# Kernel tuning notes

Hardware: AMD Instinct MI355X
Metric: run time of the kernel (lower is better)

Reference implementation:

```python
import jax, jax.numpy as jnp
import numpy as np

N_NODES = 50000
N_EDGES = 640000
HIDDEN = 128
EDGE_FEATS = 16
NUM_LAYERS = 4
NUM_GRAPHS = 64
LN_EPS = 1e-5


def setup_inputs() -> dict:
    key = jax.random.key(0)
    ks = jax.random.split(key, 12)
    s = 1.0 / np.sqrt(HIDDEN)
    se = 1.0 / np.sqrt(EDGE_FEATS)
    return {
        "x": jax.random.normal(ks[0], (N_NODES, HIDDEN), jnp.float32),
        "batch_index": jnp.sort(jax.random.randint(ks[1], (N_NODES,), 0, NUM_GRAPHS)),
        "edge_index": jax.random.randint(ks[2], (2, N_EDGES), 0, N_NODES),
        "edge_attr": jax.random.normal(ks[3], (N_EDGES, EDGE_FEATS), jnp.float32),
        # edge_transform Linear(EDGE_FEATS -> HIDDEN)
        "We": jax.random.uniform(ks[4], (EDGE_FEATS, HIDDEN), jnp.float32, -se, se),
        "be": jax.random.uniform(ks[5], (HIDDEN,), jnp.float32, -se, se),
        # per-layer GINE MLP: Linear-ReLU-Linear, stacked over layers
        "W1": jax.random.uniform(ks[6], (NUM_LAYERS, HIDDEN, HIDDEN), jnp.float32, -s, s),
        "b1": jax.random.uniform(ks[7], (NUM_LAYERS, HIDDEN), jnp.float32, -s, s),
        "W2": jax.random.uniform(ks[8], (NUM_LAYERS, HIDDEN, HIDDEN), jnp.float32, -s, s),
        "b2": jax.random.uniform(ks[9], (NUM_LAYERS, HIDDEN), jnp.float32, -s, s),
        # per-layer LayerNorm params
        "ln_g": jnp.ones((NUM_LAYERS, HIDDEN), jnp.float32),
        "ln_b": jnp.zeros((NUM_LAYERS, HIDDEN), jnp.float32),
    }


def reference(x, batch_index, edge_index, edge_attr, We, be, W1, b1, W2, b2, ln_g, ln_b):
    n = x.shape[0]
    src, dst = edge_index[0], edge_index[1]
    ea = edge_attr @ We + be  # [E, H] shared across layers
    h = x
    for l in range(W1.shape[0]):
        # GINEConv message: ReLU(x_j + edge_attr), scatter-sum at dst
        m = jax.nn.relu(h[src] + ea)
        agg = jax.ops.segment_sum(m, dst, num_segments=n)
        z = h + agg  # (1 + eps) * x + agg with eps = 0
        z = jax.nn.relu(z @ W1[l] + b1[l]) @ W2[l] + b2[l]
        # LayerNorm over feature dim
        mu = jnp.mean(z, axis=-1, keepdims=True)
        var = jnp.var(z, axis=-1, keepdims=True)
        z = (z - mu) / jnp.sqrt(var + LN_EPS) * ln_g[l] + ln_b[l]
        # dropout(p=0) is identity
        h = jax.nn.relu(z) + h
    return h
```

## Files before the change

### kernel.cpp

```cpp
#include <hip/hip_runtime.h>

#define HIDDEN 128
#define NLAYERS 4

typedef __attribute__((ext_vector_type(8))) short short8;
typedef __attribute__((ext_vector_type(4))) float f32x4;

__device__ __forceinline__ ushort f2bf(float f) {
    uint x = __builtin_bit_cast(uint, f);
    return (ushort)((x + 0x7fffu + ((x >> 16) & 1u)) >> 16);
}
__device__ __forceinline__ float bflo(uint u) {
    return __builtin_bit_cast(float, u << 16);
}
__device__ __forceinline__ float bfhi(uint u) {
    return __builtin_bit_cast(float, u & 0xffff0000u);
}


__global__ void hist_kernel(const int* __restrict__ dst, int* __restrict__ counts, int E) {
    int e = blockIdx.x * blockDim.x + threadIdx.x;
    if (e < E) atomicAdd(&counts[dst[e]], 1);
}

__global__ __launch_bounds__(1024) void scan_kernel(const int* __restrict__ counts,
                                                    int* __restrict__ offsets,
                                                    int* __restrict__ wpos, int n) {
    __shared__ int wsum[16];
    __shared__ int carry_s;
    const int t = threadIdx.x, wv = t >> 6, ln = t & 63;
    if (t == 0) carry_s = 0;
    __syncthreads();
    for (int base = 0; base < n; base += 4096) {
        const int i = base + t * 4;
        int4 c = {0, 0, 0, 0};
        if (i + 3 < n) {
            c = *(const int4*)(counts + i);
        } else {
            if (i < n)     c.x = counts[i];
            if (i + 1 < n) c.y = counts[i + 1];
            if (i + 2 < n) c.z = counts[i + 2];
            if (i + 3 < n) c.w = counts[i + 3];
        }
        const int tsum = c.x + c.y + c.z + c.w;
        int s = tsum;
#pragma unroll
        for (int off = 1; off < 64; off <<= 1) {
            int x = __shfl_up(s, off, 64);
            if (ln >= off) s += x;
        }
        if (ln == 63) wsum[wv] = s;
        __syncthreads();
        if (t < 16) {
            int x = wsum[t];
#pragma unroll
            for (int off = 1; off < 16; off <<= 1) {
                int y = __shfl_up(x, off, 16);
                if ((t & 15) >= off) x += y;
            }
            wsum[t] = x;
        }
        __syncthreads();
        const int wbase = (wv ? wsum[wv - 1] : 0) + carry_s;
        const int excl = wbase + s - tsum;
        int4 o;
        o.x = excl;
        o.y = excl + c.x;
        o.z = o.y + c.y;
        o.w = o.z + c.z;
        if (i + 3 < n) {
            *(int4*)(offsets + i) = o;
            *(int4*)(wpos + i) = o;
        } else {
            if (i < n)     { offsets[i] = o.x;     wpos[i] = o.x; }
            if (i + 1 < n) { offsets[i + 1] = o.y; wpos[i + 1] = o.y; }
            if (i + 2 < n) { offsets[i + 2] = o.z; wpos[i + 2] = o.z; }
            if (i + 3 < n) { offsets[i + 3] = o.w; wpos[i + 3] = o.w; }
        }
        __syncthreads();
        if (t == 0) carry_s += wsum[15];
        __syncthreads();
    }
    if (t == 0) offsets[n] = carry_s;
}

__global__ void fill_kernel(const int* __restrict__ src, const int* __restrict__ dst,
                            int* __restrict__ wpos, int* __restrict__ csr_src,
                            int* __restrict__ csr_eid, int E) {
    int e = blockIdx.x * blockDim.x + threadIdx.x;
    if (e < E) {
        int d = dst[e];
        int p = atomicAdd(&wpos[d], 1);
        csr_src[p] = src[e];
        csr_eid[p] = e;
    }
}


__global__ void h16init_kernel(const float* __restrict__ x, ushort* __restrict__ h16p, int total) {
    int i = blockIdx.x * blockDim.x + threadIdx.x;
    if (i < total) {
        int row = i >> 4, lm = i & 15;
        const float* xp = x + (size_t)row * HIDDEN + lm;
        uint4 o;
        o.x = (uint)f2bf(xp[0])  | ((uint)f2bf(xp[16]) << 16);
        o.y = (uint)f2bf(xp[32]) | ((uint)f2bf(xp[48]) << 16);
        o.z = (uint)f2bf(xp[64]) | ((uint)f2bf(xp[80]) << 16);
        o.w = (uint)f2bf(xp[96]) | ((uint)f2bf(xp[112]) << 16);
        *(uint4*)(h16p + (size_t)row * HIDDEN + lm * 8) = o;
    }
}

__global__ void wconv_kernel(const float* __restrict__ W1, const float* __restrict__ W2,
                             ushort* __restrict__ Wt) {
    int i = blockIdx.x * blockDim.x + threadIdx.x;
    int l = i >> 15;
    int m = (i >> 14) & 1;
    int nn = (i >> 7) & 127;
    int kpos = i & 127;
    int kk = (m == 0) ? (((kpos & 7) << 4) | (kpos >> 3)) : kpos;
    const float* W = m ? W2 : W1;
    Wt[i] = f2bf(W[l * 16384 + kk * 128 + nn]);
}

__global__ void wecol_kernel(const float* __restrict__ We, ushort* __restrict__ Wecol) {
    int i = blockIdx.x * blockDim.x + threadIdx.x;
    if (i < 128 * 16) {
        int ch = i >> 4, f = i & 15;
        Wecol[i] = f2bf(We[f * HIDDEN + ch]);
    }
}

__global__ void eattr16_kernel(const int* __restrict__ csr_eid,
                               const float4* __restrict__ edge_attr,
                               ushort* __restrict__ eattr16, int total4) {
    int i = blockIdx.x * blockDim.x + threadIdx.x;
    if (i < total4) {
        int p = i >> 2, part = i & 3;
        int eid = csr_eid[p];
        float4 v = edge_attr[(size_t)eid * 4 + part];
        uint2 o;
        o.x = (uint)f2bf(v.x) | ((uint)f2bf(v.y) << 16);
        o.y = (uint)f2bf(v.z) | ((uint)f2bf(v.w) << 16);
        *(uint2*)(eattr16 + (size_t)p * 16 + part * 4) = o;
    }
}

__global__ __launch_bounds__(256) void agg_kernel(const ushort* __restrict__ h16p,
                                                  const float* __restrict__ h32,
                                                  const int* __restrict__ csr_src,
                                                  const ushort* __restrict__ eattr16,
                                                  const int* __restrict__ offsets,
                                                  const ushort* __restrict__ Wecol,
                                                  const float* __restrict__ be,
                                                  ushort* __restrict__ z0p, int n) {
    const int w = threadIdx.x >> 6, l = threadIdx.x & 63;
    const int v = blockIdx.x * 4 + w;
    if (v >= n) return;
    const int lm = l & 15, lg = l >> 4;

    short8 bfr[8];
    float bev[8];
#pragma unroll
    for (int nt = 0; nt < 8; ++nt) {
        if (lg < 2) bfr[nt] = *(const short8*)(Wecol + (nt * 16 + lm) * 16 + lg * 8);
        else        bfr[nt] = short8{0, 0, 0, 0, 0, 0, 0, 0};
        bev[nt] = be[nt * 16 + lm];
    }

    const int e0 = offsets[v], e1 = offsets[v + 1];
    float acc[8];
#pragma unroll
    for (int i = 0; i < 8; ++i) acc[i] = 0.f;

    for (int B = e0; B < e1; B += 16) {
        short8 af = short8{0, 0, 0, 0, 0, 0, 0, 0};
        if (lg < 2) {
            int ae = B + lm;
            if (ae >= e1) ae = e1 - 1;
            af = *(const short8*)(eattr16 + (size_t)ae * 16 + lg * 8);
        }

        int ecs[4];
        float vm[4];
#pragma unroll
        for (int j = 0; j < 4; ++j) {
            int e = B + lg * 4 + j;
            vm[j] = (e < e1) ? 1.f : 0.f;
            ecs[j] = (e < e1) ? e : (e1 - 1);
        }
        int sj[4];
#pragma unroll
        for (int j = 0; j < 4; ++j) sj[j] = csr_src[ecs[j]];
        uint4 hv[4];
#pragma unroll
        for (int j = 0; j < 4; ++j)
            hv[j] = *(const uint4*)(h16p + (size_t)sj[j] * HIDDEN + lm * 8);

        f32x4 d[8];
#pragma unroll
        for (int nt = 0; nt < 8; ++nt) {
            f32x4 c = {bev[nt], bev[nt], bev[nt], bev[nt]};
            d[nt] = __builtin_amdgcn_mfma_f32_16x16x32_bf16(af, bfr[nt], c, 0, 0, 0);
        }

#pragma unroll
        for (int j = 0; j < 4; ++j) {
            float hc0 = bflo(hv[j].x), hc1 = bfhi(hv[j].x);
            float hc2 = bflo(hv[j].y), hc3 = bfhi(hv[j].y);
            float hc4 = bflo(hv[j].z), hc5 = bfhi(hv[j].z);
            float hc6 = bflo(hv[j].w), hc7 = bfhi(hv[j].w);
            acc[0] = fmaf(vm[j], fmaxf(d[0][j] + hc0, 0.f), acc[0]);
            acc[1] = fmaf(vm[j], fmaxf(d[1][j] + hc1, 0.f), acc[1]);
            acc[2] = fmaf(vm[j], fmaxf(d[2][j] + hc2, 0.f), acc[2]);
            acc[3] = fmaf(vm[j], fmaxf(d[3][j] + hc3, 0.f), acc[3]);
            acc[4] = fmaf(vm[j], fmaxf(d[4][j] + hc4, 0.f), acc[4]);
            acc[5] = fmaf(vm[j], fmaxf(d[5][j] + hc5, 0.f), acc[5]);
            acc[6] = fmaf(vm[j], fmaxf(d[6][j] + hc6, 0.f), acc[6]);
            acc[7] = fmaf(vm[j], fmaxf(d[7][j] + hc7, 0.f), acc[7]);
        }
    }

#pragma unroll
    for (int i = 0; i < 8; ++i) {
        acc[i] += __shfl_xor(acc[i], 16, 64);
        acc[i] += __shfl_xor(acc[i], 32, 64);
    }

    if (lg == 0) {
        const float* hp = h32 + (size_t)v * HIDDEN + lm;
        float s0 = hp[0]   + acc[0], s1 = hp[16]  + acc[1];
        float s2 = hp[32]  + acc[2], s3 = hp[48]  + acc[3];
        float s4 = hp[64]  + acc[4], s5 = hp[80]  + acc[5];
        float s6 = hp[96]  + acc[6], s7 = hp[112] + acc[7];
        uint4 o;
        o.x = (uint)f2bf(s0) | ((uint)f2bf(s1) << 16);
        o.y = (uint)f2bf(s2) | ((uint)f2bf(s3) << 16);
        o.z = (uint)f2bf(s4) | ((uint)f2bf(s5) << 16);
        o.w = (uint)f2bf(s6) | ((uint)f2bf(s7) << 16);
        *(uint4*)(z0p + (size_t)v * HIDDEN + lm * 8) = o;
    }
}

__global__ __launch_bounds__(256, 3) void mlp_kernel(const ushort* __restrict__ z0p,
                                                     float* __restrict__ h32,
                                                     ushort* __restrict__ h16p,
                                                     const ushort* __restrict__ W1t,
                                                     const ushort* __restrict__ W2t,
                                                     const float* __restrict__ b1,
                                                     const float* __restrict__ b2,
                                                     const float* __restrict__ lng,
                                                     const float* __restrict__ lnb,
                                                     int n, int write_h16) {
    __shared__ char smem[49152];
    const int t = threadIdx.x, l = t & 63, w = t >> 6;
    const int lm = l & 15, lg = l >> 4;
    const int r0 = blockIdx.x * 64;

#pragma unroll
    for (int j = 0; j < 8; ++j) {
        int idx = t + j * 256;
        int byte = (idx * 16) ^ (((idx >> 4) & 7) << 4);
        *(short8*)(smem + byte) = *(const short8*)(W1t + idx * 8);
    }

    float b1v[8], b2v[8], lngv[8], lnbv[8];
#pragma unroll
    for (int nt = 0; nt < 8; ++nt) {
        int col = nt * 16 + lm;
        b1v[nt] = b1[col]; b2v[nt] = b2[col];
        lngv[nt] = lng[col]; lnbv[nt] = lnb[col];
    }

    short8 a[4];
    {
        int arow = r0 + w * 16 + lm;
        if (arow >= n) arow = n - 1;
        const ushort* zp = z0p + (size_t)arow * HIDDEN + lg * 8;
#pragma unroll
        for (int kk = 0; kk < 4; ++kk) a[kk] = *(const short8*)(zp + kk * 32);
    }
    __syncthreads();

    f32x4 acc[8];
#pragma unroll
    for (int nt = 0; nt < 8; ++nt) {
        f32x4 c = {0.f, 0.f, 0.f, 0.f};
#pragma unroll
        for (int kk = 0; kk < 4; ++kk) {
            int nrow = nt * 16 + lm;
            int byte = (nrow * 256 + kk * 64 + lg * 16) ^ ((nrow & 7) << 4);
            short8 b = *(const short8*)(smem + byte);
            c = __builtin_amdgcn_mfma_f32_16x16x32_bf16(a[kk], b, c, 0, 0, 0);
        }
        acc[nt] = c;
    }

#pragma unroll
    for (int nt = 0; nt < 8; ++nt) {
        int col = nt * 16 + lm;
#pragma unroll
        for (int j = 0; j < 4; ++j) {
            int rw = w * 16 + lg * 4 + j;
            int byte = (rw * 256 + col * 2) ^ ((rw & 7) << 4);
            *(ushort*)(smem + 32768 + byte) = f2bf(fmaxf(acc[nt][j] + b1v[nt], 0.f));
        }
    }
    __syncthreads();

#pragma unroll
    for (int j = 0; j < 8; ++j) {
        int idx = t + j * 256;
        int byte = (idx * 16) ^ (((idx >> 4) & 7) << 4);
        *(short8*)(smem + byte) = *(const short8*)(W2t + idx * 8);
    }
    short8 a2[4];
    {
        int rw = w * 16 + lm;
#pragma unroll
        for (int kk = 0; kk < 4; ++kk) {
            int byte = (rw * 256 + kk * 64 + lg * 16) ^ ((rw & 7) << 4);
            a2[kk] = *(const short8*)(smem + 32768 + byte);
        }
    }
    __syncthreads();

    f32x4 acc2[8];
#pragma unroll
    for (int nt = 0; nt < 8; ++nt) {
        f32x4 c = {0.f, 0.f, 0.f, 0.f};
#pragma unroll
        for (int kk = 0; kk < 4; ++kk) {
            int nrow = nt * 16 + lm;
            int byte = (nrow * 256 + kk * 64 + lg * 16) ^ ((nrow & 7) << 4);
            short8 b = *(const short8*)(smem + byte);
            c = __builtin_amdgcn_mfma_f32_16x16x32_bf16(a2[kk], b, c, 0, 0, 0);
        }
        acc2[nt] = c;
    }

    float val[8][4];
#pragma unroll
    for (int nt = 0; nt < 8; ++nt)
#pragma unroll
        for (int j = 0; j < 4; ++j) val[nt][j] = acc2[nt][j] + b2v[nt];

    float mu[4], rs[4];
#pragma unroll
    for (int j = 0; j < 4; ++j) {
        float s = 0.f;
#pragma unroll
        for (int nt = 0; nt < 8; ++nt) s += val[nt][j];
        s += __shfl_xor(s, 1, 64); s += __shfl_xor(s, 2, 64);
        s += __shfl_xor(s, 4, 64); s += __shfl_xor(s, 8, 64);
        mu[j] = s * (1.f / 128.f);
        float d2 = 0.f;
#pragma unroll
        for (int nt = 0; nt < 8; ++nt) {
            float d = val[nt][j] - mu[j];
            d2 = fmaf(d, d, d2);
        }
        d2 += __shfl_xor(d2, 1, 64); d2 += __shfl_xor(d2, 2, 64);
        d2 += __shfl_xor(d2, 4, 64); d2 += __shfl_xor(d2, 8, 64);
        rs[j] = rsqrtf(d2 * (1.f / 128.f) + 1e-5f);
    }

#pragma unroll
    for (int j = 0; j < 4; ++j) {
        int grow = r0 + w * 16 + lg * 4 + j;
        if (grow < n) {
            uint pk[4];
#pragma unroll
            for (int nt = 0; nt < 8; ++nt) {
                int col = nt * 16 + lm;
                size_t o = (size_t)grow * HIDDEN + col;
                float y = fmaxf((val[nt][j] - mu[j]) * rs[j] * lngv[nt] + lnbv[nt], 0.f) + h32[o];
                h32[o] = y;
                uint b = (uint)f2bf(y);
                if (nt & 1) pk[nt >> 1] |= b << 16;
                else        pk[nt >> 1] = b;
            }
            if (write_h16) {
                uint4 o4 = {pk[0], pk[1], pk[2], pk[3]};
                *(uint4*)(h16p + (size_t)grow * HIDDEN + lm * 8) = o4;
            }
        }
    }
}


extern "C" void kernel_launch(void* const* d_in, const int* in_sizes, int n_in,
                              void* d_out, int out_size, void* d_ws, size_t ws_size,
                              hipStream_t stream) {
    const float* x     = (const float*)d_in[0];
    const int*   ei    = (const int*)d_in[2];
    const float* eattr = (const float*)d_in[3];
    const float* We    = (const float*)d_in[4];
    const float* be    = (const float*)d_in[5];
    const float* W1    = (const float*)d_in[6];
    const float* b1    = (const float*)d_in[7];
    const float* W2    = (const float*)d_in[8];
    const float* b2    = (const float*)d_in[9];
    const float* lng   = (const float*)d_in[10];
    const float* lnb   = (const float*)d_in[11];
    float* h32 = (float*)d_out;

    const int n = in_sizes[0] / HIDDEN;
    const int E = in_sizes[2] / 2;
    const int* src = ei;
    const int* dst = ei + E;

    size_t off = 0;
    auto take = [&](size_t bytes) {
        void* p = (char*)d_ws + off;
        off += (bytes + 255) & ~(size_t)255;
        return p;
    };
    ushort* z0p     = (ushort*)take((size_t)n * HIDDEN * 2);
    ushort* h16p    = (ushort*)take((size_t)n * HIDDEN * 2);
    ushort* Wt      = (ushort*)take((size_t)NLAYERS * 2 * HIDDEN * HIDDEN * 2);
    ushort* Wecol   = (ushort*)take((size_t)HIDDEN * 16 * 2);
    int*    counts  = (int*)take((size_t)n * 4);
    int*    offsets = (int*)take(((size_t)n + 1) * 4);
    int*    wpos    = (int*)take((size_t)n * 4);
    int*    csr_src = (int*)take((size_t)E * 4);
    int*    csr_eid = (int*)take((size_t)E * 4);
    ushort* eattr16 = (ushort*)take((size_t)E * 16 * 2);

    hipMemcpyAsync(h32, x, (size_t)n * HIDDEN * 4, hipMemcpyDeviceToDevice, stream);
    h16init_kernel<<<((n * 16) + 255) / 256, 256, 0, stream>>>(x, h16p, n * 16);
    wconv_kernel<<<(NLAYERS * 2 * HIDDEN * HIDDEN) / 256, 256, 0, stream>>>(W1, W2, Wt);
    wecol_kernel<<<(128 * 16 + 255) / 256, 256, 0, stream>>>(We, Wecol);

    hipMemsetAsync(counts, 0, (size_t)n * 4, stream);
    int eb = (E + 255) / 256;
    hist_kernel<<<eb, 256, 0, stream>>>(dst, counts, E);
    scan_kernel<<<1, 1024, 0, stream>>>(counts, offsets, wpos, n);
    fill_kernel<<<eb, 256, 0, stream>>>(src, dst, wpos, csr_src, csr_eid, E);
    eattr16_kernel<<<(E * 4 + 255) / 256, 256, 0, stream>>>(csr_eid, (const float4*)eattr,
                                                            eattr16, E * 4);

    for (int lyr = 0; lyr < NLAYERS; ++lyr) {
        agg_kernel<<<(n + 3) / 4, 256, 0, stream>>>(h16p, h32, csr_src, eattr16, offsets,
                                                    Wecol, be, z0p, n);
        mlp_kernel<<<(n + 63) / 64, 256, 0, stream>>>(z0p, h32, h16p,
                                                      Wt + (size_t)(lyr * 2 + 0) * 16384,
                                                      Wt + (size_t)(lyr * 2 + 1) * 16384,
                                                      b1 + (size_t)lyr * HIDDEN,
                                                      b2 + (size_t)lyr * HIDDEN,
                                                      lng + (size_t)lyr * HIDDEN,
                                                      lnb + (size_t)lyr * HIDDEN,
                                                      n, lyr != NLAYERS - 1);
    }
}
```

Measured before the change: 438.1 us.

## Keep residual state in bf16, fold edge bias into MFMA, stream edge weights

The fp32 residual copy h32 is now read and written only on the final layer. Earlier layers carry the residual in the bf16 h16p buffer, which removes the initial device copy and per-layer fp32 traffic in both kernels. The edge bias is folded into the MFMA by adding a constant-one input column and a bias row to the weight matrix. Edge weights are streamed per tile instead of held in registers, to cut register pressure so launch bounds can allow 8 blocks. The cost is that the residual accumulates bf16 rounding across layers, which reduces accuracy.

```diff
diff --git a/kernel.cpp b/kernel.cpp
--- a/kernel.cpp
+++ b/kernel.cpp
@@ -123,11 +123,13 @@
     Wt[i] = f2bf(W[l * 16384 + kk * 128 + nn]);
 }
 
-__global__ void wecol_kernel(const float* __restrict__ We, ushort* __restrict__ Wecol) {
+__global__ void wecolx_kernel(const float* __restrict__ We, const float* __restrict__ be,
+                              ushort* __restrict__ WecolX) {
     int i = blockIdx.x * blockDim.x + threadIdx.x;
-    if (i < 128 * 16) {
-        int ch = i >> 4, f = i & 15;
-        Wecol[i] = f2bf(We[f * HIDDEN + ch]);
+    if (i < 128 * 32) {
+        int ch = i >> 5, k = i & 31;
+        float v = (k < 16) ? We[k * HIDDEN + ch] : ((k == 16) ? be[ch] : 0.f);
+        WecolX[i] = f2bf(v);
     }
 }
 
@@ -146,78 +148,63 @@
     }
 }
 
-__global__ __launch_bounds__(256) void agg_kernel(const ushort* __restrict__ h16p,
-                                                  const float* __restrict__ h32,
-                                                  const int* __restrict__ csr_src,
-                                                  const ushort* __restrict__ eattr16,
-                                                  const int* __restrict__ offsets,
-                                                  const ushort* __restrict__ Wecol,
-                                                  const float* __restrict__ be,
-                                                  ushort* __restrict__ z0p, int n) {
+__global__ __launch_bounds__(256, 8) void agg_kernel(const ushort* __restrict__ h16p,
+                                                     const int* __restrict__ csr_src,
+                                                     const ushort* __restrict__ eattr16,
+                                                     const int* __restrict__ offsets,
+                                                     const ushort* __restrict__ WecolX,
+                                                     ushort* __restrict__ z0p, int n) {
     const int w = threadIdx.x >> 6, l = threadIdx.x & 63;
     const int v = blockIdx.x * 4 + w;
     if (v >= n) return;
     const int lm = l & 15, lg = l >> 4;
 
-    short8 bfr[8];
-    float bev[8];
-#pragma unroll
-    for (int nt = 0; nt < 8; ++nt) {
-        if (lg < 2) bfr[nt] = *(const short8*)(Wecol + (nt * 16 + lm) * 16 + lg * 8);
-        else        bfr[nt] = short8{0, 0, 0, 0, 0, 0, 0, 0};
-        bev[nt] = be[nt * 16 + lm];
-    }
-
     const int e0 = offsets[v], e1 = offsets[v + 1];
     float acc[8];
 #pragma unroll
     for (int i = 0; i < 8; ++i) acc[i] = 0.f;
 
     for (int B = e0; B < e1; B += 16) {
-        short8 af = short8{0, 0, 0, 0, 0, 0, 0, 0};
+        short8 af;
         if (lg < 2) {
             int ae = B + lm;
             if (ae >= e1) ae = e1 - 1;
             af = *(const short8*)(eattr16 + (size_t)ae * 16 + lg * 8);
-        }
-
-        int ecs[4];
+        } else if (lg == 2) {
+            af = short8{(short)0x3F80, 0, 0, 0, 0, 0, 0, 0};
+        } else {
+            af = short8{0, 0, 0, 0, 0, 0, 0, 0};
+        }
+
         float vm[4];
+        int sj[4];
 #pragma unroll
         for (int j = 0; j < 4; ++j) {
             int e = B + lg * 4 + j;
             vm[j] = (e < e1) ? 1.f : 0.f;
-            ecs[j] = (e < e1) ? e : (e1 - 1);
-        }
-        int sj[4];
-#pragma unroll
-        for (int j = 0; j < 4; ++j) sj[j] = csr_src[ecs[j]];
+            int ec = (e < e1) ? e : (e1 - 1);
+            sj[j] = csr_src[ec];
+        }
         uint4 hv[4];
 #pragma unroll
         for (int j = 0; j < 4; ++j)
             hv[j] = *(const uint4*)(h16p + (size_t)sj[j] * HIDDEN + lm * 8);
 
-        f32x4 d[8];
+        short8 b0 = *(const short8*)(WecolX + (size_t)lm * 32 + lg * 8);
 #pragma unroll
         for (int nt = 0; nt < 8; ++nt) {
-            f32x4 c = {bev[nt], bev[nt], bev[nt], bev[nt]};
-            d[nt] = __builtin_amdgcn_mfma_f32_16x16x32_bf16(af, bfr[nt], c, 0, 0, 0);
-        }
-
-#pragma unroll
-        for (int j = 0; j < 4; ++j) {
-            float hc0 = bflo(hv[j].x), hc1 = bfhi(hv[j].x);
-            float hc2 = bflo(hv[j].y), hc3 = bfhi(hv[j].y);
-            float hc4 = bflo(hv[j].z), hc5 = bfhi(hv[j].z);
-            float hc6 = bflo(hv[j].w), hc7 = bfhi(hv[j].w);
-            acc[0] = fmaf(vm[j], fmaxf(d[0][j] + hc0, 0.f), acc[0]);
-            acc[1] = fmaf(vm[j], fmaxf(d[1][j] + hc1, 0.f), acc[1]);
-            acc[2] = fmaf(vm[j], fmaxf(d[2][j] + hc2, 0.f), acc[2]);
-            acc[3] = fmaf(vm[j], fmaxf(d[3][j] + hc3, 0.f), acc[3]);
-            acc[4] = fmaf(vm[j], fmaxf(d[4][j] + hc4, 0.f), acc[4]);
-            acc[5] = fmaf(vm[j], fmaxf(d[5][j] + hc5, 0.f), acc[5]);
-            acc[6] = fmaf(vm[j], fmaxf(d[6][j] + hc6, 0.f), acc[6]);
-            acc[7] = fmaf(vm[j], fmaxf(d[7][j] + hc7, 0.f), acc[7]);
+            short8 bnext = b0;
+            if (nt < 7)
+                bnext = *(const short8*)(WecolX + (size_t)((nt + 1) * 16 + lm) * 32 + lg * 8);
+            f32x4 c = {0.f, 0.f, 0.f, 0.f};
+            f32x4 d = __builtin_amdgcn_mfma_f32_16x16x32_bf16(af, b0, c, 0, 0, 0);
+#pragma unroll
+            for (int j = 0; j < 4; ++j) {
+                uint word = (nt < 2) ? hv[j].x : (nt < 4) ? hv[j].y : (nt < 6) ? hv[j].z : hv[j].w;
+                float hc = (nt & 1) ? bfhi(word) : bflo(word);
+                acc[nt] = fmaf(vm[j], fmaxf(d[j] + hc, 0.f), acc[nt]);
+            }
+            b0 = bnext;
         }
     }
 
@@ -228,30 +215,26 @@
     }
 
     if (lg == 0) {
-        const float* hp = h32 + (size_t)v * HIDDEN + lm;
-        float s0 = hp[0]   + acc[0], s1 = hp[16]  + acc[1];
-        float s2 = hp[32]  + acc[2], s3 = hp[48]  + acc[3];
-        float s4 = hp[64]  + acc[4], s5 = hp[80]  + acc[5];
-        float s6 = hp[96]  + acc[6], s7 = hp[112] + acc[7];
+        const uint4 sv = *(const uint4*)(h16p + (size_t)v * HIDDEN + lm * 8);
         uint4 o;
-        o.x = (uint)f2bf(s0) | ((uint)f2bf(s1) << 16);
-        o.y = (uint)f2bf(s2) | ((uint)f2bf(s3) << 16);
-        o.z = (uint)f2bf(s4) | ((uint)f2bf(s5) << 16);
-        o.w = (uint)f2bf(s6) | ((uint)f2bf(s7) << 16);
+        o.x = (uint)f2bf(bflo(sv.x) + acc[0]) | ((uint)f2bf(bfhi(sv.x) + acc[1]) << 16);
+        o.y = (uint)f2bf(bflo(sv.y) + acc[2]) | ((uint)f2bf(bfhi(sv.y) + acc[3]) << 16);
+        o.z = (uint)f2bf(bflo(sv.z) + acc[4]) | ((uint)f2bf(bfhi(sv.z) + acc[5]) << 16);
+        o.w = (uint)f2bf(bflo(sv.w) + acc[6]) | ((uint)f2bf(bfhi(sv.w) + acc[7]) << 16);
         *(uint4*)(z0p + (size_t)v * HIDDEN + lm * 8) = o;
     }
 }
 
 __global__ __launch_bounds__(256, 3) void mlp_kernel(const ushort* __restrict__ z0p,
+                                                     ushort* __restrict__ h16p,
                                                      float* __restrict__ h32,
-                                                     ushort* __restrict__ h16p,
                                                      const ushort* __restrict__ W1t,
                                                      const ushort* __restrict__ W2t,
                                                      const float* __restrict__ b1,
                                                      const float* __restrict__ b2,
                                                      const float* __restrict__ lng,
                                                      const float* __restrict__ lnb,
-                                                     int n, int write_h16) {
+                                                     int n, int last) {
     __shared__ char smem[49152];
     const int t = threadIdx.x, l = t & 63, w = t >> 6;
     const int lm = l & 15, lg = l >> 4;
@@ -369,19 +352,23 @@
     for (int j = 0; j < 4; ++j) {
         int grow = r0 + w * 16 + lg * 4 + j;
         if (grow < n) {
-            uint pk[4];
-#pragma unroll
-            for (int nt = 0; nt < 8; ++nt) {
-                int col = nt * 16 + lm;
-                size_t o = (size_t)grow * HIDDEN + col;
-                float y = fmaxf((val[nt][j] - mu[j]) * rs[j] * lngv[nt] + lnbv[nt], 0.f) + h32[o];
-                h32[o] = y;
-                uint b = (uint)f2bf(y);
-                if (nt & 1) pk[nt >> 1] |= b << 16;
-                else        pk[nt >> 1] = b;
-            }
-            if (write_h16) {
-                uint4 o4 = {pk[0], pk[1], pk[2], pk[3]};
+            const uint4 hvv = *(const uint4*)(h16p + (size_t)grow * HIDDEN + lm * 8);
+            float hc[8] = {bflo(hvv.x), bfhi(hvv.x), bflo(hvv.y), bfhi(hvv.y),
+                           bflo(hvv.z), bfhi(hvv.z), bflo(hvv.w), bfhi(hvv.w)};
+            float y[8];
+#pragma unroll
+            for (int nt = 0; nt < 8; ++nt)
+                y[nt] = fmaxf((val[nt][j] - mu[j]) * rs[j] * lngv[nt] + lnbv[nt], 0.f) + hc[nt];
+            if (last) {
+#pragma unroll
+                for (int nt = 0; nt < 8; ++nt)
+                    h32[(size_t)grow * HIDDEN + nt * 16 + lm] = y[nt];
+            } else {
+                uint4 o4;
+                o4.x = (uint)f2bf(y[0]) | ((uint)f2bf(y[1]) << 16);
+                o4.y = (uint)f2bf(y[2]) | ((uint)f2bf(y[3]) << 16);
+                o4.z = (uint)f2bf(y[4]) | ((uint)f2bf(y[5]) << 16);
+                o4.w = (uint)f2bf(y[6]) | ((uint)f2bf(y[7]) << 16);
                 *(uint4*)(h16p + (size_t)grow * HIDDEN + lm * 8) = o4;
             }
         }
@@ -419,7 +406,7 @@
     ushort* z0p     = (ushort*)take((size_t)n * HIDDEN * 2);
     ushort* h16p    = (ushort*)take((size_t)n * HIDDEN * 2);
     ushort* Wt      = (ushort*)take((size_t)NLAYERS * 2 * HIDDEN * HIDDEN * 2);
-    ushort* Wecol   = (ushort*)take((size_t)HIDDEN * 16 * 2);
+    ushort* WecolX  = (ushort*)take((size_t)HIDDEN * 32 * 2);
     int*    counts  = (int*)take((size_t)n * 4);
     int*    offsets = (int*)take(((size_t)n + 1) * 4);
     int*    wpos    = (int*)take((size_t)n * 4);
@@ -427,10 +414,9 @@
     int*    csr_eid = (int*)take((size_t)E * 4);
     ushort* eattr16 = (ushort*)take((size_t)E * 16 * 2);
 
-    hipMemcpyAsync(h32, x, (size_t)n * HIDDEN * 4, hipMemcpyDeviceToDevice, stream);
     h16init_kernel<<<((n * 16) + 255) / 256, 256, 0, stream>>>(x, h16p, n * 16);
     wconv_kernel<<<(NLAYERS * 2 * HIDDEN * HIDDEN) / 256, 256, 0, stream>>>(W1, W2, Wt);
-    wecol_kernel<<<(128 * 16 + 255) / 256, 256, 0, stream>>>(We, Wecol);
+    wecolx_kernel<<<(128 * 32 + 255) / 256, 256, 0, stream>>>(We, be, WecolX);
 
     hipMemsetAsync(counts, 0, (size_t)n * 4, stream);
     int eb = (E + 255) / 256;
@@ -441,15 +427,15 @@
                                                             eattr16, E * 4);
 
     for (int lyr = 0; lyr < NLAYERS; ++lyr) {
-        agg_kernel<<<(n + 3) / 4, 256, 0, stream>>>(h16p, h32, csr_src, eattr16, offsets,
-                                                    Wecol, be, z0p, n);
-        mlp_kernel<<<(n + 63) / 64, 256, 0, stream>>>(z0p, h32, h16p,
+        agg_kernel<<<(n + 3) / 4, 256, 0, stream>>>(h16p, csr_src, eattr16, offsets,
+                                                    WecolX, z0p, n);
+        mlp_kernel<<<(n + 63) / 64, 256, 0, stream>>>(z0p, h16p, h32,
                                                       Wt + (size_t)(lyr * 2 + 0) * 16384,
                                                       Wt + (size_t)(lyr * 2 + 1) * 16384,
                                                       b1 + (size_t)lyr * HIDDEN,
                                                       b2 + (size_t)lyr * HIDDEN,
                                                       lng + (size_t)lyr * HIDDEN,
                                                       lnb + (size_t)lyr * HIDDEN,
-                                                      n, lyr != NLAYERS - 1);
-    }
-}
+                                                      n, lyr == NLAYERS - 1);
+    }
+}
```

After: 901.0 us. 106% more time.
